# Optimization experiments

Measured on AMD Instinct MI355X. Metric: run time of the kernel, lower is better.

The kernel has to match this reference:

```python
import jax, jax.numpy as jnp
import numpy as np

LN_EPS = 1e-5


def _sage_mean(x, Wl, bl, src, dst, ew, n_nodes):
    # lin_l then gather-weight-scatter mean: out[i] = mean_{j->i} ew * (x[j] @ Wl + bl)
    h = x @ Wl + bl                                  # [N, D]
    msg = h[src] * ew[:, None]                       # [E, D] gather + scale
    s = jax.ops.segment_sum(msg, dst, num_segments=n_nodes)          # [N, D]
    cnt = jax.ops.segment_sum(jnp.ones_like(ew), dst, num_segments=n_nodes)
    return s / jnp.maximum(cnt, 1.0)[:, None]


def _layernorm(x, gamma, beta):
    mu = jnp.mean(x, axis=-1, keepdims=True)
    var = jnp.var(x, axis=-1, keepdims=True)
    return (x - mu) * jax.lax.rsqrt(var + LN_EPS) * gamma + beta


def setup_inputs() -> dict:
    key = jax.random.key(0)
    ks = jax.random.split(key, 8)
    N, E, D = 50000, 800000, 128
    x = jax.random.normal(ks[0], (N, D), dtype=jnp.float32)
    edge_index = jax.random.randint(ks[1], (2, E), 0, N, dtype=jnp.int64)
    edge_weight = jax.random.uniform(ks[2], (E,), dtype=jnp.float32)
    sc = 1.0 / np.sqrt(D)
    Wl1 = jax.random.normal(ks[3], (D, D), dtype=jnp.float32) * sc
    bl1 = jnp.zeros((D,), dtype=jnp.float32)
    Wl2 = jax.random.normal(ks[4], (D, D), dtype=jnp.float32) * sc
    bl2 = jnp.zeros((D,), dtype=jnp.float32)
    gamma = jnp.ones((D,), dtype=jnp.float32)
    beta = jnp.zeros((D,), dtype=jnp.float32)
    return {"x": x, "edge_index": edge_index, "edge_weight": edge_weight,
            "Wl1": Wl1, "bl1": bl1, "Wl2": Wl2, "bl2": bl2,
            "gamma": gamma, "beta": beta}


def reference(x, edge_index, edge_weight, Wl1, bl1, Wl2, bl2, gamma, beta):
    N = x.shape[0]
    src, dst = edge_index[0], edge_index[1]
    # Layer 1: WeightedSAGEConv (no self-loops; update() returns aggr only)
    x1 = _sage_mean(x, Wl1, bl1, src, dst, edge_weight, N)
    # Layer 2: ResGraphConv — residual is Identity (in==out), add self-loops w=1
    loops = jnp.arange(N, dtype=edge_index.dtype)
    src2 = jnp.concatenate([src, loops])
    dst2 = jnp.concatenate([dst, loops])
    ew2 = jnp.concatenate([edge_weight, jnp.ones((N,), dtype=edge_weight.dtype)])
    out = _sage_mean(x1, Wl2, bl2, src2, dst2, ew2, N)
    out = _layernorm(out + x1, gamma, beta)
    return jax.nn.gelu(out, approximate=False)
```

## Files before the change

kernel.cpp:

```cpp
#include <hip/hip_runtime.h>
#include <math.h>

#define DF 128
#define NPB 256
#define EPB 4096
#define CAP 7168

typedef __attribute__((ext_vector_type(8))) short bf16x8;
typedef __attribute__((ext_vector_type(4))) float f32x4;

__device__ __forceinline__ float bf2f(uint u) {
    union { uint i; float f; } v; v.i = u << 16; return v.f;
}
__device__ __forceinline__ uint f2bf(float f) {
    union { float f; uint i; } v; v.f = f;
    return (v.i + 0x7fffu + ((v.i >> 16) & 1u)) >> 16;
}


__global__ void prep_k(const float* __restrict__ x, uint* __restrict__ xb, int n4,
                       const float* __restrict__ W1, const float* __restrict__ W2,
                       uint* __restrict__ Wt1, uint* __restrict__ Wt2,
                       const int* __restrict__ dst, int* __restrict__ cnt, int E,
                       int cvtxB) {
    int b = blockIdx.x;
    if (b < cvtxB) {
        int i = b * 256 + threadIdx.x;
        if (i < n4) {
            float4 v = ((const float4*)x)[i];
            uint2 o;
            o.x = f2bf(v.x) | (f2bf(v.y) << 16);
            o.y = f2bf(v.z) | (f2bf(v.w) << 16);
            ((uint2*)xb)[i] = o;
        }
    } else if (b < cvtxB + 64) {
        int i = (b - cvtxB) * 256 + threadIdx.x;
        const float* W = (i < 8192) ? W1 : W2;
        uint* Wt = (i < 8192) ? Wt1 : Wt2;
        int j = i & 8191;
        int n = j >> 6, kk = j & 63;
        Wt[n * 64 + kk] = f2bf(W[(2 * kk) * DF + n]) | (f2bf(W[(2 * kk + 1) * DF + n]) << 16);
    } else {
        int e0 = ((b - cvtxB - 64) * 256 + threadIdx.x) * 4;
        if (e0 + 4 <= E) {
            int4 d = *(const int4*)(dst + e0);
            atomicAdd(&cnt[d.x], 1);
            atomicAdd(&cnt[d.y], 1);
            atomicAdd(&cnt[d.z], 1);
            atomicAdd(&cnt[d.w], 1);
        } else {
            for (int j = e0; j < E; ++j) atomicAdd(&cnt[dst[j]], 1);
        }
    }
}


__global__ void partial_k(const int* __restrict__ cnt, int* __restrict__ bsum, int N) {
    int t = threadIdx.x, b = blockIdx.x;
    int base = b * 1024 + t * 4;
    int s = 0;
    if (base + 4 <= N) {
        int4 v = *(const int4*)(cnt + base);
        s = v.x + v.y + v.z + v.w;
    } else {
        for (int j = 0; j < 4; ++j)
            if (base + j < N) s += cnt[base + j];
    }
    __shared__ int sm[256];
    sm[t] = s;
    __syncthreads();
    for (int off = 128; off > 0; off >>= 1) {
        if (t < off) sm[t] += sm[t + off];
        __syncthreads();
    }
    if (t == 0) bsum[b] = sm[0];
}

__global__ void scanb_k(const int* __restrict__ bsum, int* __restrict__ boff,
                        int* __restrict__ rowptr, int nb, int N) {
    int t = threadIdx.x;
    int v = (t < nb) ? bsum[t] : 0;
    __shared__ int sm[256];
    sm[t] = v;
    __syncthreads();
    for (int off = 1; off < 256; off <<= 1) {
        int u = (t >= off) ? sm[t - off] : 0;
        __syncthreads();
        sm[t] += u;
        __syncthreads();
    }
    if (t < nb) boff[t] = sm[t] - v;
    if (t == 255) rowptr[N] = sm[255];
}

__global__ void rowfill_k(const int* __restrict__ cnt, const int* __restrict__ boff,
                          int* __restrict__ rowptr, int* __restrict__ cursor, int N) {
    int t = threadIdx.x, b = blockIdx.x;
    int base = b * 1024 + t * 4;
    int c0 = 0, c1 = 0, c2 = 0, c3 = 0;
    if (base + 4 <= N) {
        int4 v = *(const int4*)(cnt + base);
        c0 = v.x; c1 = v.y; c2 = v.z; c3 = v.w;
    } else {
        if (base + 0 < N) c0 = cnt[base + 0];
        if (base + 1 < N) c1 = cnt[base + 1];
        if (base + 2 < N) c2 = cnt[base + 2];
        if (base + 3 < N) c3 = cnt[base + 3];
    }
    int s = c0 + c1 + c2 + c3;
    __shared__ int sm[256];
    sm[t] = s;
    __syncthreads();
    for (int off = 1; off < 256; off <<= 1) {
        int u = (t >= off) ? sm[t - off] : 0;
        __syncthreads();
        sm[t] += u;
        __syncthreads();
    }
    int run = boff[b] + sm[t] - s;
    if (base + 0 < N) { rowptr[base + 0] = run; cursor[base + 0] = run; run += c0; }
    if (base + 1 < N) { rowptr[base + 1] = run; cursor[base + 1] = run; run += c1; }
    if (base + 2 < N) { rowptr[base + 2] = run; cursor[base + 2] = run; run += c2; }
    if (base + 3 < N) { rowptr[base + 3] = run; cursor[base + 3] = run; run += c3; }
}

__global__ void gcinit_k(const int* __restrict__ rowptr, int* __restrict__ gcur, int nbk) {
    int b = threadIdx.x;
    if (b < nbk) gcur[b] = rowptr[b * NPB];
}

__global__ __launch_bounds__(256) void passA_k(
    const int* __restrict__ src, const int* __restrict__ dst,
    const float* __restrict__ ew, int* __restrict__ gcur,
    uint2* __restrict__ stage, int E) {
    __shared__ int lhist[256];
    __shared__ int lscan[256];
    __shared__ int lcur[256];
    __shared__ int gbase[256];
    __shared__ unsigned char lbk[EPB];
    __shared__ uint2 img[EPB];
    int t = threadIdx.x;
    int base = blockIdx.x * EPB;
    int cnt = min(EPB, E - base);
    lhist[t] = 0;
    __syncthreads();
    uint ps[16], pw[16];
    int pb[16];
#pragma unroll
    for (int k = 0; k < 16; ++k) {
        int i = base + k * 256 + t;
        pb[k] = -1;
        if (i < E) {
            int d = dst[i];
            int bk = d >> 8;
            pb[k] = bk;
            ps[k] = (uint)src[i] | ((uint)(d & 255) << 23);
            pw[k] = __float_as_uint(ew[i]);
            atomicAdd(&lhist[bk], 1);
        }
    }
    __syncthreads();
    int v = lhist[t];
    lscan[t] = v;
    __syncthreads();
    for (int off = 1; off < 256; off <<= 1) {
        int u = (t >= off) ? lscan[t - off] : 0;
        __syncthreads();
        lscan[t] += u;
        __syncthreads();
    }
    lcur[t] = lscan[t] - v;
    if (v > 0) gbase[t] = atomicAdd(&gcur[t], v);
    __syncthreads();
#pragma unroll
    for (int k = 0; k < 16; ++k) {
        if (pb[k] >= 0) {
            int p = atomicAdd(&lcur[pb[k]], 1);
            img[p] = make_uint2(ps[k], pw[k]);
            lbk[p] = (unsigned char)pb[k];
        }
    }
    __syncthreads();
    for (int i = t; i < cnt; i += 256) {
        int bk = lbk[i];
        stage[gbase[bk] + (i - (lscan[bk] - lhist[bk]))] = img[i];
    }
}

__global__ __launch_bounds__(256) void passB_k(
    const uint2* __restrict__ stage, const int* __restrict__ rowptr,
    int* __restrict__ cursor, int2* __restrict__ adj, int N) {
    __shared__ int lcur[256];
    __shared__ uint2 img[CAP];
    int t = threadIdx.x;
    int b = blockIdx.x;
    int nb0 = b * NPB;
    int nn = min(NPB, N - nb0);
    int ebase = rowptr[nb0];
    int ecnt = rowptr[nb0 + nn] - ebase;
    if (t < nn) lcur[t] = rowptr[nb0 + t] - ebase;
    __syncthreads();
    if (ecnt <= CAP) {
        for (int i = t; i < ecnt; i += 256) {
            uint2 e = stage[ebase + i];
            int dl = (e.x >> 23) & 255;
            int p = atomicAdd(&lcur[dl], 1);
            img[p] = make_uint2(e.x & 0x7fffffu, e.y);
        }
        __syncthreads();
        for (int i = t; i < ecnt; i += 256) {
            uint2 e = img[i];
            adj[ebase + i] = make_int2((int)e.x, (int)e.y);
        }
    } else {
        for (int i = t; i < ecnt; i += 256) {
            uint2 e = stage[ebase + i];
            int dl = (e.x >> 23) & 255;
            int p = atomicAdd(&cursor[nb0 + dl], 1);
            adj[p] = make_int2((int)(e.x & 0x7fffffu), (int)e.y);
        }
    }
}

__global__ void fill_k(const int* __restrict__ src, const int* __restrict__ dst,
                       const float* __restrict__ ew, int* __restrict__ cursor,
                       int2* __restrict__ adj, int E) {
    int i = blockIdx.x * blockDim.x + threadIdx.x;
    if (i < E) {
        int p = atomicAdd(&cursor[dst[i]], 1);
        int2 e;
        e.x = src[i];
        e.y = __float_as_int(ew[i]);
        adj[p] = e;
    }
}


template <int SELF>
__global__ void agg_k(const uint* __restrict__ xb, const int* __restrict__ rowptr,
                      const int2* __restrict__ adj, uint* __restrict__ aggb,
                      float* __restrict__ sumew, int N) {
    int wid = (blockIdx.x * blockDim.x + threadIdx.x) >> 6;
    int lane = threadIdx.x & 63;
    if (wid >= N) return;
    int lo = rowptr[wid], hi = rowptr[wid + 1];
    float a0 = 0.f, a1 = 0.f, ws = 0.f;
    if (SELF) {
        uint v = xb[(size_t)wid * 64 + lane];
        a0 = bf2f(v & 0xffffu);
        a1 = bf2f(v >> 16);
    }
    for (int base = lo; base < hi; base += 64) {
        int p = base + lane;
        int sidx = 0; float wv = 0.f;
        if (p < hi) {
            int2 e = adj[p];
            sidx = e.x;
            wv = __int_as_float(e.y);
        }
        ws += wv;
        int cnt = min(hi - base, 64);
        int j = 0;
        for (; j + 8 <= cnt; j += 8) {
            int s0 = __shfl(sidx, j),     s1 = __shfl(sidx, j + 1);
            int s2 = __shfl(sidx, j + 2), s3 = __shfl(sidx, j + 3);
            int s4 = __shfl(sidx, j + 4), s5 = __shfl(sidx, j + 5);
            int s6 = __shfl(sidx, j + 6), s7 = __shfl(sidx, j + 7);
            float w0 = __shfl(wv, j),     w1 = __shfl(wv, j + 1);
            float w2 = __shfl(wv, j + 2), w3 = __shfl(wv, j + 3);
            float w4 = __shfl(wv, j + 4), w5 = __shfl(wv, j + 5);
            float w6 = __shfl(wv, j + 6), w7 = __shfl(wv, j + 7);
            uint v0 = xb[(size_t)s0 * 64 + lane];
            uint v1 = xb[(size_t)s1 * 64 + lane];
            uint v2 = xb[(size_t)s2 * 64 + lane];
            uint v3 = xb[(size_t)s3 * 64 + lane];
            uint v4 = xb[(size_t)s4 * 64 + lane];
            uint v5 = xb[(size_t)s5 * 64 + lane];
            uint v6 = xb[(size_t)s6 * 64 + lane];
            uint v7 = xb[(size_t)s7 * 64 + lane];
            a0 += w0 * bf2f(v0 & 0xffffu); a1 += w0 * bf2f(v0 >> 16);
            a0 += w1 * bf2f(v1 & 0xffffu); a1 += w1 * bf2f(v1 >> 16);
            a0 += w2 * bf2f(v2 & 0xffffu); a1 += w2 * bf2f(v2 >> 16);
            a0 += w3 * bf2f(v3 & 0xffffu); a1 += w3 * bf2f(v3 >> 16);
            a0 += w4 * bf2f(v4 & 0xffffu); a1 += w4 * bf2f(v4 >> 16);
            a0 += w5 * bf2f(v5 & 0xffffu); a1 += w5 * bf2f(v5 >> 16);
            a0 += w6 * bf2f(v6 & 0xffffu); a1 += w6 * bf2f(v6 >> 16);
            a0 += w7 * bf2f(v7 & 0xffffu); a1 += w7 * bf2f(v7 >> 16);
        }
        for (; j < cnt; ++j) {
            int sj = __shfl(sidx, j);
            float wj = __shfl(wv, j);
            uint v = xb[(size_t)sj * 64 + lane];
            a0 += wj * bf2f(v & 0xffffu);
            a1 += wj * bf2f(v >> 16);
        }
    }
    if (!SELF) {
        ws += __shfl_xor(ws, 1);
        ws += __shfl_xor(ws, 2);
        ws += __shfl_xor(ws, 4);
        ws += __shfl_xor(ws, 8);
        ws += __shfl_xor(ws, 16);
        ws += __shfl_xor(ws, 32);
        if (lane == 0) sumew[wid] = ws;
    }
    float inv = SELF ? 1.0f / (float)(hi - lo + 1)
                     : 1.0f / fmaxf((float)(hi - lo), 1.0f);
    aggb[(size_t)wid * 64 + lane] = f2bf(a0 * inv) | (f2bf(a1 * inv) << 16);
}


__global__ __launch_bounds__(256) void mm1_k(
    const ushort* __restrict__ aggb, const ushort* __restrict__ Wt,
    const float* __restrict__ bl, const float* __restrict__ sumew,
    const int* __restrict__ rowptr, ushort* __restrict__ x1b, int N) {
    int lane = threadIdx.x & 63;
    int strip = blockIdx.x * 4 + (threadIdx.x >> 6);
    int nstrips = (N + 15) >> 4;
    if (strip >= nstrips) return;
    int row0 = strip << 4;
    int arow = row0 + (lane & 15);
    if (arow >= N) arow = N - 1;
    int kg = (lane >> 4) << 3;
    int bcol = lane & 15;

    bf16x8 af[4];
#pragma unroll
    for (int kc = 0; kc < 4; ++kc)
        af[kc] = *(const bf16x8*)(aggb + (size_t)arow * DF + kc * 32 + kg);

    f32x4 acc[8];
#pragma unroll
    for (int nt = 0; nt < 8; ++nt) {
        f32x4 a = {0.f, 0.f, 0.f, 0.f};
#pragma unroll
        for (int kc = 0; kc < 4; ++kc) {
            bf16x8 bf = *(const bf16x8*)(Wt + (size_t)(nt * 16 + bcol) * DF + kc * 32 + kg);
            a = __builtin_amdgcn_mfma_f32_16x16x32_bf16(af[kc], bf, a, 0, 0, 0);
        }
        acc[nt] = a;
    }

#pragma unroll
    for (int r = 0; r < 4; ++r) {
        int R = row0 + ((lane >> 4) << 2) + r;
        if (R >= N) continue;
        int deg = rowptr[R + 1] - rowptr[R];
        float wb = sumew[R] / fmaxf((float)deg, 1.0f);
#pragma unroll
        for (int nt = 0; nt < 8; ++nt) {
            int col = nt * 16 + bcol;
            x1b[(size_t)R * DF + col] = (ushort)f2bf(acc[nt][r] + bl[col] * wb);
        }
    }
}

__device__ __forceinline__ float gelu_exact(float v) {
    return 0.5f * v * (1.0f + erff(v * 0.70710678118654752440f));
}

__global__ __launch_bounds__(256) void mm2_k(
    const ushort* __restrict__ aggb, const ushort* __restrict__ Wt,
    const float* __restrict__ bl, const float* __restrict__ sumew,
    const int* __restrict__ rowptr, const ushort* __restrict__ x1b,
    const float* __restrict__ gamma, const float* __restrict__ beta,
    float* __restrict__ out, int N) {
    int lane = threadIdx.x & 63;
    int strip = blockIdx.x * 4 + (threadIdx.x >> 6);
    int nstrips = (N + 15) >> 4;
    if (strip >= nstrips) return;
    int row0 = strip << 4;
    int arow = row0 + (lane & 15);
    if (arow >= N) arow = N - 1;
    int kg = (lane >> 4) << 3;
    int bcol = lane & 15;

    bf16x8 af[4];
#pragma unroll
    for (int kc = 0; kc < 4; ++kc)
        af[kc] = *(const bf16x8*)(aggb + (size_t)arow * DF + kc * 32 + kg);

    f32x4 acc[8];
#pragma unroll
    for (int nt = 0; nt < 8; ++nt) {
        f32x4 a = {0.f, 0.f, 0.f, 0.f};
#pragma unroll
        for (int kc = 0; kc < 4; ++kc) {
            bf16x8 bf = *(const bf16x8*)(Wt + (size_t)(nt * 16 + bcol) * DF + kc * 32 + kg);
            a = __builtin_amdgcn_mfma_f32_16x16x32_bf16(af[kc], bf, a, 0, 0, 0);
        }
        acc[nt] = a;
    }

#pragma unroll
    for (int r = 0; r < 4; ++r) {
        int R = row0 + ((lane >> 4) << 2) + r;
        if (R >= N) continue;
        int deg = rowptr[R + 1] - rowptr[R];
        float wb = (sumew[R] + 1.0f) / (float)(deg + 1);
        float pre[8];
        float s = 0.f;
#pragma unroll
        for (int nt = 0; nt < 8; ++nt) {
            int col = nt * 16 + bcol;
            pre[nt] = acc[nt][r] + bl[col] * wb + bf2f(x1b[(size_t)R * DF + col]);
            s += pre[nt];
        }
        s += __shfl_xor(s, 1);
        s += __shfl_xor(s, 2);
        s += __shfl_xor(s, 4);
        s += __shfl_xor(s, 8);
        float mu = s * (1.0f / 128.0f);
        float vs = 0.f;
#pragma unroll
        for (int nt = 0; nt < 8; ++nt) {
            float d = pre[nt] - mu;
            vs += d * d;
        }
        vs += __shfl_xor(vs, 1);
        vs += __shfl_xor(vs, 2);
        vs += __shfl_xor(vs, 4);
        vs += __shfl_xor(vs, 8);
        float rstd = rsqrtf(vs * (1.0f / 128.0f) + 1e-5f);
#pragma unroll
        for (int nt = 0; nt < 8; ++nt) {
            int col = nt * 16 + bcol;
            float y = (pre[nt] - mu) * rstd * gamma[col] + beta[col];
            out[(size_t)R * DF + col] = gelu_exact(y);
        }
    }
}


extern "C" void kernel_launch(void* const* d_in, const int* in_sizes, int n_in,
                              void* d_out, int out_size, void* d_ws, size_t ws_size,
                              hipStream_t stream) {
    const float* x     = (const float*)d_in[0];
    const int*   ei    = (const int*)d_in[1];
    const float* ew    = (const float*)d_in[2];
    const float* Wl1   = (const float*)d_in[3];
    const float* bl1   = (const float*)d_in[4];
    const float* Wl2   = (const float*)d_in[5];
    const float* bl2   = (const float*)d_in[6];
    const float* gamma = (const float*)d_in[7];
    const float* beta  = (const float*)d_in[8];
    float* out = (float*)d_out;

    int N = in_sizes[0] / DF;
    int E = in_sizes[2];
    const int* src = ei;
    const int* dst = ei + E;

    char* ws = (char*)d_ws;
    size_t off = 0;
    auto alloc = [&](size_t bytes) -> void* {
        void* p = ws + off;
        off += (bytes + 255) & ~(size_t)255;
        return p;
    };
    int*    cnt     = (int*)alloc((size_t)N * 4);
    float*  sumew   = (float*)alloc((size_t)N * 4);
    int*    rowptr  = (int*)alloc((size_t)(N + 1) * 4);
    int*    cursor  = (int*)alloc((size_t)N * 4);
    int*    bsum    = (int*)alloc(1024);
    int*    boff    = (int*)alloc(1024);
    int*    gcur    = (int*)alloc(1024);
    int2*   adj     = (int2*)alloc((size_t)E * 8);
    uint2*  stage   = (uint2*)alloc((size_t)E * 8);
    uint*   xb      = (uint*)alloc((size_t)N * DF * 2);
    uint*   aggb    = (uint*)alloc((size_t)N * DF * 2);
    ushort* x1b     = (ushort*)alloc((size_t)N * DF * 2);
    uint*   Wt1     = (uint*)alloc((size_t)DF * DF * 2);
    uint*   Wt2     = (uint*)alloc((size_t)DF * DF * 2);

    hipMemsetAsync(cnt, 0, (size_t)N * 4, stream);

    int n4 = N * DF / 4;
    int cvtxB = (n4 + 255) / 256;
    int histB = (E + 1023) / 1024;
    hipLaunchKernelGGL(prep_k, dim3(cvtxB + 64 + histB), dim3(256), 0, stream,
                       x, xb, n4, Wl1, Wl2, Wt1, Wt2, dst, cnt, E, cvtxB);

    int nb_scan = (N + 1023) / 1024;
    hipLaunchKernelGGL(partial_k, dim3(nb_scan), dim3(256), 0, stream, cnt, bsum, N);
    hipLaunchKernelGGL(scanb_k, dim3(1), dim3(256), 0, stream, bsum, boff, rowptr, nb_scan, N);
    hipLaunchKernelGGL(rowfill_k, dim3(nb_scan), dim3(256), 0, stream, cnt, boff, rowptr, cursor, N);

    int nbk = (N + NPB - 1) / NPB;
    if (nbk <= 256) {
        hipLaunchKernelGGL(gcinit_k, dim3(1), dim3(256), 0, stream, rowptr, gcur, nbk);
        int ab = (E + EPB - 1) / EPB;
        hipLaunchKernelGGL(passA_k, dim3(ab), dim3(256), 0, stream, src, dst, ew, gcur, stage, E);
        hipLaunchKernelGGL(passB_k, dim3(nbk), dim3(256), 0, stream, stage, rowptr, cursor, adj, N);
    } else {
        int eb = (E + 255) / 256;
        hipLaunchKernelGGL(fill_k, dim3(eb), dim3(256), 0, stream, src, dst, ew, cursor, adj, E);
    }

    int nb = (N * 64 + 255) / 256;
    int nstrips = (N + 15) / 16;
    int mb = (nstrips + 3) / 4;

    hipLaunchKernelGGL(agg_k<0>, dim3(nb), dim3(256), 0, stream, xb, rowptr, adj, aggb, sumew, N);
    hipLaunchKernelGGL(mm1_k, dim3(mb), dim3(256), 0, stream,
                       (const ushort*)aggb, (const ushort*)Wt1, bl1, sumew, rowptr, x1b, N);
    hipLaunchKernelGGL(agg_k<1>, dim3(nb), dim3(256), 0, stream, (const uint*)x1b, rowptr, adj, aggb, sumew, N);
    hipLaunchKernelGGL(mm2_k, dim3(mb), dim3(256), 0, stream,
                       (const ushort*)aggb, (const ushort*)Wt2, bl2, sumew, rowptr, x1b, gamma, beta, out, N);
}
```

Baseline: 204.5 us.

## Replace per-node count histogram and scan with coarse bucket histogram

The CSR build no longer computes a per-node degree histogram with global atomics followed by a three-kernel scan. Instead, prep builds a 196-bucket histogram (dst>>8) in shared memory, one small kernel scans it, and passB derives per-node row pointers from a local histogram of its bucket's staged edges. This removes the N-sized memset, 800K global atomics and two launches. The cost is an extra read of the staged edges inside passB. The old path is kept for large N.

```diff
diff --git a/kernel.cpp b/kernel.cpp
--- a/kernel.cpp
+++ b/kernel.cpp
@@ -21,11 +21,13 @@
 __global__ void prep_k(const float* __restrict__ x, uint* __restrict__ xb, int n4,
                        const float* __restrict__ W1, const float* __restrict__ W2,
                        uint* __restrict__ Wt1, uint* __restrict__ Wt2,
-                       const int* __restrict__ dst, int* __restrict__ cnt, int E,
+                       const int* __restrict__ dst, int* __restrict__ bcnt, int E,
                        int cvtxB) {
+    __shared__ int lh[256];
     int b = blockIdx.x;
+    int t = threadIdx.x;
     if (b < cvtxB) {
-        int i = b * 256 + threadIdx.x;
+        int i = b * 256 + t;
         if (i < n4) {
             float4 v = ((const float4*)x)[i];
             uint2 o;
@@ -34,52 +36,31 @@
             ((uint2*)xb)[i] = o;
         }
     } else if (b < cvtxB + 64) {
-        int i = (b - cvtxB) * 256 + threadIdx.x;
+        int i = (b - cvtxB) * 256 + t;
         const float* W = (i < 8192) ? W1 : W2;
         uint* Wt = (i < 8192) ? Wt1 : Wt2;
         int j = i & 8191;
         int n = j >> 6, kk = j & 63;
         Wt[n * 64 + kk] = f2bf(W[(2 * kk) * DF + n]) | (f2bf(W[(2 * kk + 1) * DF + n]) << 16);
     } else {
-        int e0 = ((b - cvtxB - 64) * 256 + threadIdx.x) * 4;
-        if (e0 + 4 <= E) {
-            int4 d = *(const int4*)(dst + e0);
-            atomicAdd(&cnt[d.x], 1);
-            atomicAdd(&cnt[d.y], 1);
-            atomicAdd(&cnt[d.z], 1);
-            atomicAdd(&cnt[d.w], 1);
-        } else {
-            for (int j = e0; j < E; ++j) atomicAdd(&cnt[dst[j]], 1);
-        }
-    }
-}
-
-
-__global__ void partial_k(const int* __restrict__ cnt, int* __restrict__ bsum, int N) {
-    int t = threadIdx.x, b = blockIdx.x;
-    int base = b * 1024 + t * 4;
-    int s = 0;
-    if (base + 4 <= N) {
-        int4 v = *(const int4*)(cnt + base);
-        s = v.x + v.y + v.z + v.w;
-    } else {
-        for (int j = 0; j < 4; ++j)
-            if (base + j < N) s += cnt[base + j];
-    }
-    __shared__ int sm[256];
-    sm[t] = s;
-    __syncthreads();
-    for (int off = 128; off > 0; off >>= 1) {
-        if (t < off) sm[t] += sm[t + off];
-        __syncthreads();
-    }
-    if (t == 0) bsum[b] = sm[0];
-}
-
-__global__ void scanb_k(const int* __restrict__ bsum, int* __restrict__ boff,
-                        int* __restrict__ rowptr, int nb, int N) {
+        int base = (b - cvtxB - 64) * EPB;
+        lh[t] = 0;
+        __syncthreads();
+#pragma unroll
+        for (int k = 0; k < EPB / 256; ++k) {
+            int i = base + k * 256 + t;
+            if (i < E) atomicAdd(&lh[dst[i] >> 8], 1);
+        }
+        __syncthreads();
+        int v = lh[t];
+        if (v) atomicAdd(&bcnt[t], v);
+    }
+}
+
+__global__ void bscan_k(const int* __restrict__ bcnt, int* __restrict__ bkoff,
+                        int* __restrict__ gcur) {
     int t = threadIdx.x;
-    int v = (t < nb) ? bsum[t] : 0;
+    int v = bcnt[t];
     __shared__ int sm[256];
     sm[t] = v;
     __syncthreads();
@@ -89,44 +70,10 @@
         sm[t] += u;
         __syncthreads();
     }
-    if (t < nb) boff[t] = sm[t] - v;
-    if (t == 255) rowptr[N] = sm[255];
-}
-
-__global__ void rowfill_k(const int* __restrict__ cnt, const int* __restrict__ boff,
-                          int* __restrict__ rowptr, int* __restrict__ cursor, int N) {
-    int t = threadIdx.x, b = blockIdx.x;
-    int base = b * 1024 + t * 4;
-    int c0 = 0, c1 = 0, c2 = 0, c3 = 0;
-    if (base + 4 <= N) {
-        int4 v = *(const int4*)(cnt + base);
-        c0 = v.x; c1 = v.y; c2 = v.z; c3 = v.w;
-    } else {
-        if (base + 0 < N) c0 = cnt[base + 0];
-        if (base + 1 < N) c1 = cnt[base + 1];
-        if (base + 2 < N) c2 = cnt[base + 2];
-        if (base + 3 < N) c3 = cnt[base + 3];
-    }
-    int s = c0 + c1 + c2 + c3;
-    __shared__ int sm[256];
-    sm[t] = s;
-    __syncthreads();
-    for (int off = 1; off < 256; off <<= 1) {
-        int u = (t >= off) ? sm[t - off] : 0;
-        __syncthreads();
-        sm[t] += u;
-        __syncthreads();
-    }
-    int run = boff[b] + sm[t] - s;
-    if (base + 0 < N) { rowptr[base + 0] = run; cursor[base + 0] = run; run += c0; }
-    if (base + 1 < N) { rowptr[base + 1] = run; cursor[base + 1] = run; run += c1; }
-    if (base + 2 < N) { rowptr[base + 2] = run; cursor[base + 2] = run; run += c2; }
-    if (base + 3 < N) { rowptr[base + 3] = run; cursor[base + 3] = run; run += c3; }
-}
-
-__global__ void gcinit_k(const int* __restrict__ rowptr, int* __restrict__ gcur, int nbk) {
-    int b = threadIdx.x;
-    if (b < nbk) gcur[b] = rowptr[b * NPB];
+    int ex = sm[t] - v;
+    bkoff[t] = ex;
+    gcur[t] = ex;
+    if (t == 255) bkoff[256] = sm[255];
 }
 
 __global__ __launch_bounds__(256) void passA_k(
@@ -188,23 +135,47 @@
 }
 
 __global__ __launch_bounds__(256) void passB_k(
-    const uint2* __restrict__ stage, const int* __restrict__ rowptr,
-    int* __restrict__ cursor, int2* __restrict__ adj, int N) {
+    const uint2* __restrict__ stage, const int* __restrict__ bkoff,
+    int* __restrict__ rowptr, int* __restrict__ cursor,
+    int2* __restrict__ adj, int N, int nbk) {
+    __shared__ int lhist[256];
+    __shared__ int lpre[256];
     __shared__ int lcur[256];
     __shared__ uint2 img[CAP];
     int t = threadIdx.x;
     int b = blockIdx.x;
     int nb0 = b * NPB;
     int nn = min(NPB, N - nb0);
-    int ebase = rowptr[nb0];
-    int ecnt = rowptr[nb0 + nn] - ebase;
-    if (t < nn) lcur[t] = rowptr[nb0 + t] - ebase;
+    int ebase = bkoff[b];
+    int ecnt = bkoff[b + 1] - ebase;
+    lhist[t] = 0;
+    __syncthreads();
+    for (int i = t; i < ecnt; i += 256) {
+        uint2 e = stage[ebase + i];
+        atomicAdd(&lhist[(e.x >> 23) & 255], 1);
+    }
+    __syncthreads();
+    int v = lhist[t];
+    lpre[t] = v;
+    __syncthreads();
+    for (int off = 1; off < 256; off <<= 1) {
+        int u = (t >= off) ? lpre[t - off] : 0;
+        __syncthreads();
+        lpre[t] += u;
+        __syncthreads();
+    }
+    int myoff = lpre[t] - v;
+    lcur[t] = myoff;
+    if (t < nn) {
+        rowptr[nb0 + t] = ebase + myoff;
+        cursor[nb0 + t] = ebase + myoff;
+    }
+    if (b == nbk - 1 && t == 0) rowptr[N] = ebase + ecnt;
     __syncthreads();
     if (ecnt <= CAP) {
         for (int i = t; i < ecnt; i += 256) {
             uint2 e = stage[ebase + i];
-            int dl = (e.x >> 23) & 255;
-            int p = atomicAdd(&lcur[dl], 1);
+            int p = atomicAdd(&lcur[(e.x >> 23) & 255], 1);
             img[p] = make_uint2(e.x & 0x7fffffu, e.y);
         }
         __syncthreads();
@@ -220,6 +191,81 @@
             adj[p] = make_int2((int)(e.x & 0x7fffffu), (int)e.y);
         }
     }
+}
+
+
+__global__ void histn_k(const int* __restrict__ dst, int* __restrict__ cnt, int E) {
+    int i = blockIdx.x * blockDim.x + threadIdx.x;
+    if (i < E) atomicAdd(&cnt[dst[i]], 1);
+}
+
+__global__ void partial_k(const int* __restrict__ cnt, int* __restrict__ bsum, int N) {
+    int t = threadIdx.x, b = blockIdx.x;
+    int base = b * 1024 + t * 4;
+    int s = 0;
+    if (base + 4 <= N) {
+        int4 v = *(const int4*)(cnt + base);
+        s = v.x + v.y + v.z + v.w;
+    } else {
+        for (int j = 0; j < 4; ++j)
+            if (base + j < N) s += cnt[base + j];
+    }
+    __shared__ int sm[256];
+    sm[t] = s;
+    __syncthreads();
+    for (int off = 128; off > 0; off >>= 1) {
+        if (t < off) sm[t] += sm[t + off];
+        __syncthreads();
+    }
+    if (t == 0) bsum[b] = sm[0];
+}
+
+__global__ void scanb_k(const int* __restrict__ bsum, int* __restrict__ boff,
+                        int* __restrict__ rowptr, int nb, int N) {
+    int t = threadIdx.x;
+    int v = (t < nb) ? bsum[t] : 0;
+    __shared__ int sm[256];
+    sm[t] = v;
+    __syncthreads();
+    for (int off = 1; off < 256; off <<= 1) {
+        int u = (t >= off) ? sm[t - off] : 0;
+        __syncthreads();
+        sm[t] += u;
+        __syncthreads();
+    }
+    if (t < nb) boff[t] = sm[t] - v;
+    if (t == 255) rowptr[N] = sm[255];
+}
+
+__global__ void rowfill_k(const int* __restrict__ cnt, const int* __restrict__ boff,
+                          int* __restrict__ rowptr, int* __restrict__ cursor, int N) {
+    int t = threadIdx.x, b = blockIdx.x;
+    int base = b * 1024 + t * 4;
+    int c0 = 0, c1 = 0, c2 = 0, c3 = 0;
+    if (base + 4 <= N) {
+        int4 v = *(const int4*)(cnt + base);
+        c0 = v.x; c1 = v.y; c2 = v.z; c3 = v.w;
+    } else {
+        if (base + 0 < N) c0 = cnt[base + 0];
+        if (base + 1 < N) c1 = cnt[base + 1];
+        if (base + 2 < N) c2 = cnt[base + 2];
+        if (base + 3 < N) c3 = cnt[base + 3];
+    }
+    int s = c0 + c1 + c2 + c3;
+    __shared__ int sm[256];
+    sm[t] = s;
+    __syncthreads();
+    for (int off = 1; off < 256; off <<= 1) {
+        int u = (t >= off) ? sm[t - off] : 0;
+        __syncthreads();
+        sm[t] += u;
+        __syncthreads();
+    }
+    int run = boff[b] + sm[t] - s;
+    if (base + 0 < N) { rowptr[base + 0] = run; cursor[base + 0] = run; run += c0; }
+    if (base + 1 < N) { rowptr[base + 1] = run; cursor[base + 1] = run; run += c1; }
+    if (base + 2 < N) { rowptr[base + 2] = run; cursor[base + 2] = run; run += c2; }
+    if (base + 3 < N) { rowptr[base + 3] = run; cursor[base + 3] = run; run += c3; }
 }
 
 __global__ void fill_k(const int* __restrict__ src, const int* __restrict__ dst,
@@ -458,13 +504,14 @@
         off += (bytes + 255) & ~(size_t)255;
         return p;
     };
-    int*    cnt     = (int*)alloc((size_t)N * 4);
     float*  sumew   = (float*)alloc((size_t)N * 4);
     int*    rowptr  = (int*)alloc((size_t)(N + 1) * 4);
     int*    cursor  = (int*)alloc((size_t)N * 4);
+    int*    bcnt    = (int*)alloc(1024);
+    int*    bkoff   = (int*)alloc(1040);
+    int*    gcur    = (int*)alloc(1024);
     int*    bsum    = (int*)alloc(1024);
     int*    boff    = (int*)alloc(1024);
-    int*    gcur    = (int*)alloc(1024);
     int2*   adj     = (int2*)alloc((size_t)E * 8);
     uint2*  stage   = (uint2*)alloc((size_t)E * 8);
     uint*   xb      = (uint*)alloc((size_t)N * DF * 2);
@@ -472,28 +519,31 @@
     ushort* x1b     = (ushort*)alloc((size_t)N * DF * 2);
     uint*   Wt1     = (uint*)alloc((size_t)DF * DF * 2);
     uint*   Wt2     = (uint*)alloc((size_t)DF * DF * 2);
-
-    hipMemsetAsync(cnt, 0, (size_t)N * 4, stream);
-
+    int*    cnt     = (int*)alloc((size_t)N * 4);
+
+    int nbk = (N + NPB - 1) / NPB;
     int n4 = N * DF / 4;
     int cvtxB = (n4 + 255) / 256;
-    int histB = (E + 1023) / 1024;
-    hipLaunchKernelGGL(prep_k, dim3(cvtxB + 64 + histB), dim3(256), 0, stream,
-                       x, xb, n4, Wl1, Wl2, Wt1, Wt2, dst, cnt, E, cvtxB);
-
-    int nb_scan = (N + 1023) / 1024;
-    hipLaunchKernelGGL(partial_k, dim3(nb_scan), dim3(256), 0, stream, cnt, bsum, N);
-    hipLaunchKernelGGL(scanb_k, dim3(1), dim3(256), 0, stream, bsum, boff, rowptr, nb_scan, N);
-    hipLaunchKernelGGL(rowfill_k, dim3(nb_scan), dim3(256), 0, stream, cnt, boff, rowptr, cursor, N);
-
-    int nbk = (N + NPB - 1) / NPB;
+    int histB = (E + EPB - 1) / EPB;
+
     if (nbk <= 256) {
-        hipLaunchKernelGGL(gcinit_k, dim3(1), dim3(256), 0, stream, rowptr, gcur, nbk);
-        int ab = (E + EPB - 1) / EPB;
-        hipLaunchKernelGGL(passA_k, dim3(ab), dim3(256), 0, stream, src, dst, ew, gcur, stage, E);
-        hipLaunchKernelGGL(passB_k, dim3(nbk), dim3(256), 0, stream, stage, rowptr, cursor, adj, N);
+        hipMemsetAsync(bcnt, 0, 1024, stream);
+        hipLaunchKernelGGL(prep_k, dim3(cvtxB + 64 + histB), dim3(256), 0, stream,
+                           x, xb, n4, Wl1, Wl2, Wt1, Wt2, dst, bcnt, E, cvtxB);
+        hipLaunchKernelGGL(bscan_k, dim3(1), dim3(256), 0, stream, bcnt, bkoff, gcur);
+        hipLaunchKernelGGL(passA_k, dim3(histB), dim3(256), 0, stream, src, dst, ew, gcur, stage, E);
+        hipLaunchKernelGGL(passB_k, dim3(nbk), dim3(256), 0, stream,
+                           stage, bkoff, rowptr, cursor, adj, N, nbk);
     } else {
+        hipMemsetAsync(cnt, 0, (size_t)N * 4, stream);
+        hipLaunchKernelGGL(prep_k, dim3(cvtxB + 64), dim3(256), 0, stream,
+                           x, xb, n4, Wl1, Wl2, Wt1, Wt2, dst, bcnt, 0, cvtxB);
         int eb = (E + 255) / 256;
+        hipLaunchKernelGGL(histn_k, dim3(eb), dim3(256), 0, stream, dst, cnt, E);
+        int nb_scan = (N + 1023) / 1024;
+        hipLaunchKernelGGL(partial_k, dim3(nb_scan), dim3(256), 0, stream, cnt, bsum, N);
+        hipLaunchKernelGGL(scanb_k, dim3(1), dim3(256), 0, stream, bsum, boff, rowptr, nb_scan, N);
+        hipLaunchKernelGGL(rowfill_k, dim3(nb_scan), dim3(256), 0, stream, cnt, boff, rowptr, cursor, N);
         hipLaunchKernelGGL(fill_k, dim3(eb), dim3(256), 0, stream, src, dst, ew, cursor, adj, E);
     }
 
```

New measurement: 170.0 us. 1.2x faster.
